# Performance work log

Measured on AMD Instinct MI355X. Metric: run time of the kernel, lower is better.

## Reference

```python
import jax, jax.numpy as jnp
import numpy as np

B, N_SNPS, N_GENES = 16, 500000, 20000
N_NODES, N_EDGES = 600000, 320000
NF, L = 8, 2
BN_EPS = 1e-5

def bn(x, g, b):
    # eval-mode BatchNorm1d with freshly-initialized running stats (mean=0, var=1)
    return x * jax.lax.rsqrt(jnp.float32(1.0) + BN_EPS) * g + b

def gelu(x):
    return jax.nn.gelu(x, approximate=False)  # torch F.gelu default (erf)

def setup_inputs():
    key = jax.random.key(0)
    ks = iter(jax.random.split(key, 40))
    nk = lambda: next(ks)
    lin = lambda kk, i, o: jax.random.normal(kk, (i, o), jnp.float32) * 0.02
    gam = lambda kk, n: 1.0 + 0.02 * jax.random.normal(kk, (n,), jnp.float32)
    inp = {}
    inp['snp'] = jax.random.uniform(nk(), (B, N_SNPS), jnp.float32)
    inp['snp_ids'] = jax.random.randint(nk(), (N_NODES,), 0, N_SNPS)
    inp['gene_of_node'] = jnp.sort(jax.random.randint(nk(), (N_NODES,), 0, N_GENES))
    inp['edge_src'] = jax.random.randint(nk(), (N_EDGES,), 0, N_GENES)
    inp['edge_dst'] = jax.random.randint(nk(), (N_EDGES,), 0, N_GENES)
    inp['filters'] = jax.random.normal(nk(), (NF, N_SNPS), jnp.float32) * 0.001
    inp['eps'] = jnp.zeros((L,), jnp.float32)  # GIN learn_eps, init 0
    inp['W1'] = jnp.stack([lin(nk(), NF, 2 * NF) for _ in range(L)])
    inp['b1'] = jnp.zeros((L, 2 * NF), jnp.float32)
    inp['g1'] = jnp.stack([gam(nk(), 2 * NF) for _ in range(L)])
    inp['bt1'] = jnp.zeros((L, 2 * NF), jnp.float32)
    inp['W2'] = jnp.stack([lin(nk(), 2 * NF, NF) for _ in range(L)])
    inp['b2'] = jnp.zeros((L, NF), jnp.float32)
    inp['g2'] = jnp.stack([gam(nk(), NF) for _ in range(L)])
    inp['bt2'] = jnp.zeros((L, NF), jnp.float32)
    inp['Wk'] = lin(nk(), NF, NF); inp['bk'] = jnp.zeros((NF,), jnp.float32)
    inp['Wq'] = lin(nk(), NF, 1)
    inp['Wv'] = lin(nk(), NF, NF); inp['bv'] = jnp.zeros((NF,), jnp.float32)
    inp['Wp1'] = lin(nk(), NF, 64); inp['bp1'] = jnp.zeros((64,), jnp.float32)
    inp['gp1'] = gam(nk(), 64); inp['btp1'] = jnp.zeros((64,), jnp.float32)
    inp['Wp2'] = lin(nk(), 64, 16); inp['bp2'] = jnp.zeros((16,), jnp.float32)
    inp['gp2'] = gam(nk(), 16); inp['btp2'] = jnp.zeros((16,), jnp.float32)
    inp['Wp3'] = lin(nk(), 16, 1); inp['bp3'] = jnp.zeros((1,), jnp.float32)
    return inp

def reference(snp, snp_ids, gene_of_node, edge_src, edge_dst, filters, eps,
              W1, b1, g1, bt1, W2, b2, g2, bt2,
              Wk, bk, Wq, Wv, bv,
              Wp1, bp1, gp1, btp1, Wp2, bp2, gp2, btp2, Wp3, bp3):
    # snp_h[b,n,f] = snp[b,n] * filters[f,n]  (concat of per-filter einsum 'bnd,n->bnd' with d=1)
    snp_h = snp[:, :, None] * filters.T[None]                      # [B, N_SNPS, NF]
    node_h = jnp.take(snp_h, snp_ids, axis=1)                      # [B, N_NODES, NF] gather per sample
    seg_gene = lambda x: jax.ops.segment_sum(x, gene_of_node, num_segments=N_GENES)
    h = jax.vmap(seg_gene)(node_h)                                 # [B, N_GENES, NF] SNP->gene readout
    seg_edge = lambda x: jax.ops.segment_sum(jnp.take(x, edge_src, axis=0), edge_dst, num_segments=N_GENES)
    for l in range(L):
        agg = jax.vmap(seg_edge)(h)                                # GIN sum aggregation on gene graph
        z = (1.0 + eps[l]) * h + agg
        z = gelu(bn(z @ W1[l] + b1[l], g1[l], bt1[l]))
        z = z @ W2[l] + b2[l]
        h = gelu(bn(z, g2[l], bt2[l]))
    # attentive readout: w = sigmoid(Wq(key(h))); graph feature = sum_nodes(value(h) * w)
    keys = h @ Wk + bk
    w = jax.nn.sigmoid(keys @ Wq)                                  # [B, N_GENES, 1]
    v = h @ Wv + bv
    g_h = jnp.sum(v * w, axis=1)                                   # [B, NF]
    z = gelu(bn(g_h @ Wp1 + bp1, gp1, btp1))
    z = gelu(bn(z @ Wp2 + bp2, gp2, btp2))
    preds = z @ Wp3 + bp3                                          # [B, 1]
    return preds, filters, w
```

## Files before the change

### kernel.cpp

```cpp
#include <hip/hip_runtime.h>
#include <math.h>

#define NSNPS  500000
#define NGENES 20000
#define NNODES 600000
#define NEDGES 320000
#define BB     16
#define NFILT  8
#define NBLK2  5000
#define MAXDEG 64

#define BN_SCALE 0.99999500003749968f

typedef unsigned short u16;

__device__ __forceinline__ float gelu_erf(float x) {
    return 0.5f * x * (1.0f + erff(x * 0.70710678118654752f));
}
__device__ __forceinline__ float sigmoidf_(float x) {
    return 1.0f / (1.0f + expf(-x));
}
__device__ __forceinline__ u16 f2bf(float x) {
    unsigned u = __float_as_uint(x);
    u += 0x7fffu + ((u >> 16) & 1u);
    return (u16)(u >> 16);
}
__device__ __forceinline__ float bf1(u16 v)      { return __uint_as_float(((unsigned)v) << 16); }
__device__ __forceinline__ float bflo(unsigned v){ return __uint_as_float(v << 16); }
__device__ __forceinline__ float bfhi(unsigned v){ return __uint_as_float(v & 0xffff0000u); }
__device__ __forceinline__ unsigned pack2(float a, float b) {
    return (unsigned)f2bf(a) | ((unsigned)f2bf(b) << 16);
}

#define KA_NA 1954
#define KA_NB 79
__global__ __launch_bounds__(256) void kA_prep(const float* __restrict__ snp,
                                               const float* __restrict__ filters,
                                               const int* __restrict__ gene_of_node,
                                               u16* __restrict__ nodeRow,
                                               float* __restrict__ out_filt,
                                               int* __restrict__ node_off,
                                               int* __restrict__ cursor,
                                               float* __restrict__ g_h8) {
    int bid = blockIdx.x;
    int t = threadIdx.x;

    if (bid < KA_NA) {
        int n = bid * 256 + t;
        if (n < NSNPS) {
            float f0 = filters[0 * NSNPS + n], f1 = filters[1 * NSNPS + n];
            float f2 = filters[2 * NSNPS + n], f3 = filters[3 * NSNPS + n];
            float f4 = filters[4 * NSNPS + n], f5 = filters[5 * NSNPS + n];
            float f6 = filters[6 * NSNPS + n], f7 = filters[7 * NSNPS + n];
            out_filt[0 * NSNPS + n] = f0; out_filt[1 * NSNPS + n] = f1;
            out_filt[2 * NSNPS + n] = f2; out_filt[3 * NSNPS + n] = f3;
            out_filt[4 * NSNPS + n] = f4; out_filt[5 * NSNPS + n] = f5;
            out_filt[6 * NSNPS + n] = f6; out_filt[7 * NSNPS + n] = f7;
            uint4 r0, r1, r2;
            r0.x = pack2(snp[0 * (size_t)NSNPS + n],  snp[1 * (size_t)NSNPS + n]);
            r0.y = pack2(snp[2 * (size_t)NSNPS + n],  snp[3 * (size_t)NSNPS + n]);
            r0.z = pack2(snp[4 * (size_t)NSNPS + n],  snp[5 * (size_t)NSNPS + n]);
            r0.w = pack2(snp[6 * (size_t)NSNPS + n],  snp[7 * (size_t)NSNPS + n]);
            r1.x = pack2(snp[8 * (size_t)NSNPS + n],  snp[9 * (size_t)NSNPS + n]);
            r1.y = pack2(snp[10 * (size_t)NSNPS + n], snp[11 * (size_t)NSNPS + n]);
            r1.z = pack2(snp[12 * (size_t)NSNPS + n], snp[13 * (size_t)NSNPS + n]);
            r1.w = pack2(snp[14 * (size_t)NSNPS + n], snp[15 * (size_t)NSNPS + n]);
            r2.x = pack2(f0, f1); r2.y = pack2(f2, f3);
            r2.z = pack2(f4, f5); r2.w = pack2(f6, f7);
            uint4* dst = (uint4*)(nodeRow + (size_t)n * 32);
            dst[0] = r0; dst[1] = r1; dst[2] = r2;
        }
        return;
    }
    int g = (bid - KA_NA) * 256 + t;
    if (g <= NGENES) {
        int lo = 0, hi = NNODES;
        while (lo < hi) {
            int mid = (lo + hi) >> 1;
            if (gene_of_node[mid] < g) lo = mid + 1; else hi = mid;
        }
        node_off[g] = lo;
    }
    if (g < NGENES) cursor[g] = g * MAXDEG;
    if (g < 1024)   g_h8[g] = 0.0f;
}

#define KB_SCAT 1250
#define KB_GATH 5000
__global__ __launch_bounds__(256) void kB_gather(const u16* __restrict__ nodeRow,
                                                 const int* __restrict__ snp_ids,
                                                 const int* __restrict__ node_off,
                                                 const int* __restrict__ edge_src,
                                                 const int* __restrict__ edge_dst,
                                                 int* __restrict__ cursor,
                                                 int* __restrict__ csr_src,
                                                 u16* __restrict__ h_bf) {
    int bid = blockIdx.x;
    int t = threadIdx.x;
    if (bid < KB_SCAT) {
        int e = bid * 256 + t;
        if (e < NEDGES) {
            int dst = edge_dst[e];
            int p = atomicAdd(&cursor[dst], 1);
            if (p < dst * MAXDEG + MAXDEG)
                csr_src[p] = edge_src[e];
        }
        return;
    }
    int wave = t >> 6, lane = t & 63;
    int g = (bid - KB_SCAT) * 4 + wave;
    int slot = lane >> 4;
    int b = lane & 15;
    int s = node_off[g], e = node_off[g + 1];

    float acc[8];
    #pragma unroll
    for (int f = 0; f < 8; f++) acc[f] = 0.0f;

    int i = s + slot;
    for (; i + 12 < e; i += 16) {
        int id0 = snp_ids[i];
        int id1 = snp_ids[i + 4];
        int id2 = snp_ids[i + 8];
        int id3 = snp_ids[i + 12];
        const u16* r0 = nodeRow + (size_t)id0 * 32;
        const u16* r1 = nodeRow + (size_t)id1 * 32;
        const u16* r2 = nodeRow + (size_t)id2 * 32;
        const u16* r3 = nodeRow + (size_t)id3 * 32;
        float v0 = bf1(r0[b]);
        float v1 = bf1(r1[b]);
        float v2 = bf1(r2[b]);
        float v3 = bf1(r3[b]);
        uint4 F0 = *(const uint4*)(r0 + 16);
        uint4 F1 = *(const uint4*)(r1 + 16);
        uint4 F2 = *(const uint4*)(r2 + 16);
        uint4 F3 = *(const uint4*)(r3 + 16);
        acc[0] += (v0 * bflo(F0.x) + v1 * bflo(F1.x)) + (v2 * bflo(F2.x) + v3 * bflo(F3.x));
        acc[1] += (v0 * bfhi(F0.x) + v1 * bfhi(F1.x)) + (v2 * bfhi(F2.x) + v3 * bfhi(F3.x));
        acc[2] += (v0 * bflo(F0.y) + v1 * bflo(F1.y)) + (v2 * bflo(F2.y) + v3 * bflo(F3.y));
        acc[3] += (v0 * bfhi(F0.y) + v1 * bfhi(F1.y)) + (v2 * bfhi(F2.y) + v3 * bfhi(F3.y));
        acc[4] += (v0 * bflo(F0.z) + v1 * bflo(F1.z)) + (v2 * bflo(F2.z) + v3 * bflo(F3.z));
        acc[5] += (v0 * bfhi(F0.z) + v1 * bfhi(F1.z)) + (v2 * bfhi(F2.z) + v3 * bfhi(F3.z));
        acc[6] += (v0 * bflo(F0.w) + v1 * bflo(F1.w)) + (v2 * bflo(F2.w) + v3 * bflo(F3.w));
        acc[7] += (v0 * bfhi(F0.w) + v1 * bfhi(F1.w)) + (v2 * bfhi(F2.w) + v3 * bfhi(F3.w));
    }
    for (; i + 4 < e; i += 8) {
        int id0 = snp_ids[i];
        int id1 = snp_ids[i + 4];
        const u16* r0 = nodeRow + (size_t)id0 * 32;
        const u16* r1 = nodeRow + (size_t)id1 * 32;
        float v0 = bf1(r0[b]);
        float v1 = bf1(r1[b]);
        uint4 F0 = *(const uint4*)(r0 + 16);
        uint4 F1 = *(const uint4*)(r1 + 16);
        acc[0] += v0 * bflo(F0.x) + v1 * bflo(F1.x);
        acc[1] += v0 * bfhi(F0.x) + v1 * bfhi(F1.x);
        acc[2] += v0 * bflo(F0.y) + v1 * bflo(F1.y);
        acc[3] += v0 * bfhi(F0.y) + v1 * bfhi(F1.y);
        acc[4] += v0 * bflo(F0.z) + v1 * bflo(F1.z);
        acc[5] += v0 * bfhi(F0.z) + v1 * bfhi(F1.z);
        acc[6] += v0 * bflo(F0.w) + v1 * bflo(F1.w);
        acc[7] += v0 * bfhi(F0.w) + v1 * bfhi(F1.w);
    }
    if (i < e) {
        int id0 = snp_ids[i];
        const u16* r0 = nodeRow + (size_t)id0 * 32;
        float v0 = bf1(r0[b]);
        uint4 F0 = *(const uint4*)(r0 + 16);
        acc[0] += v0 * bflo(F0.x); acc[1] += v0 * bfhi(F0.x);
        acc[2] += v0 * bflo(F0.y); acc[3] += v0 * bfhi(F0.y);
        acc[4] += v0 * bflo(F0.z); acc[5] += v0 * bfhi(F0.z);
        acc[6] += v0 * bflo(F0.w); acc[7] += v0 * bfhi(F0.w);
    }
    #pragma unroll
    for (int f = 0; f < 8; f++) {
        acc[f] += __shfl_xor(acc[f], 16, 64);
        acc[f] += __shfl_xor(acc[f], 32, 64);
    }
    if (lane < 16) {
        uint4 o;
        o.x = pack2(acc[0], acc[1]); o.y = pack2(acc[2], acc[3]);
        o.z = pack2(acc[4], acc[5]); o.w = pack2(acc[6], acc[7]);
        *(uint4*)(h_bf + (size_t)g * 128 + lane * 8) = o;
    }
}

__global__ __launch_bounds__(256) void kC_gin1(const u16* __restrict__ hin,
                                               u16* __restrict__ hout,
                                               const int* __restrict__ cursor,
                                               const int* __restrict__ csr_src,
                                               const float* __restrict__ eps_l,
                                               const float* __restrict__ W1,
                                               const float* __restrict__ b1,
                                               const float* __restrict__ g1,
                                               const float* __restrict__ bt1,
                                               const float* __restrict__ W2,
                                               const float* __restrict__ b2,
                                               const float* __restrict__ g2,
                                               const float* __restrict__ bt2) {
    __shared__ float sW1[128], sb1[16], sg1[16], sbt1[16];
    __shared__ float sW2[128], sb2[8], sg2[8], sbt2[8];
    int t = threadIdx.x;
    if (t < 128) { sW1[t] = W1[t]; sW2[t] = W2[t]; }
    if (t < 16)  { sb1[t] = b1[t]; sg1[t] = g1[t]; sbt1[t] = bt1[t]; }
    if (t < 8)   { sb2[t] = b2[t]; sg2[t] = g2[t]; sbt2[t] = bt2[t]; }

    int chunk = blockIdx.x & 3;
    int g = (blockIdx.x >> 2) * 16 + (t >> 4);
    int u = t & 15;
    int half = u >> 3;
    int colpos = u & 7;
    int fh = colpos & 1;
    int jgroup = half * 2 + fh;
    int col = chunk * 32 + colpos * 4;
    const u16* __restrict__ hc = hin + col;
    float epsv = 1.0f + eps_l[0];

    float a0, a1, a2, a3;
    if (half == 0) {
        uint2 su = *(const uint2*)(hc + (size_t)g * 128);
        a0 = bflo(su.x) * epsv; a1 = bfhi(su.x) * epsv;
        a2 = bflo(su.y) * epsv; a3 = bfhi(su.y) * epsv;
    } else {
        a0 = a1 = a2 = a3 = 0.0f;
    }

    int s = g * MAXDEG;
    int e = cursor[g];
    e = (e < s + MAXDEG) ? e : (s + MAXDEG);
    int k = s + half;
    for (; k + 14 < e; k += 16) {
        int i0 = csr_src[k],      i1 = csr_src[k + 2];
        int i2 = csr_src[k + 4],  i3 = csr_src[k + 6];
        int i4 = csr_src[k + 8],  i5 = csr_src[k + 10];
        int i6 = csr_src[k + 12], i7 = csr_src[k + 14];
        uint2 v0 = *(const uint2*)(hc + (size_t)i0 * 128);
        uint2 v1 = *(const uint2*)(hc + (size_t)i1 * 128);
        uint2 v2 = *(const uint2*)(hc + (size_t)i2 * 128);
        uint2 v3 = *(const uint2*)(hc + (size_t)i3 * 128);
        uint2 v4 = *(const uint2*)(hc + (size_t)i4 * 128);
        uint2 v5 = *(const uint2*)(hc + (size_t)i5 * 128);
        uint2 v6 = *(const uint2*)(hc + (size_t)i6 * 128);
        uint2 v7 = *(const uint2*)(hc + (size_t)i7 * 128);
        a0 += ((bflo(v0.x) + bflo(v1.x)) + (bflo(v2.x) + bflo(v3.x)))
            + ((bflo(v4.x) + bflo(v5.x)) + (bflo(v6.x) + bflo(v7.x)));
        a1 += ((bfhi(v0.x) + bfhi(v1.x)) + (bfhi(v2.x) + bfhi(v3.x)))
            + ((bfhi(v4.x) + bfhi(v5.x)) + (bfhi(v6.x) + bfhi(v7.x)));
        a2 += ((bflo(v0.y) + bflo(v1.y)) + (bflo(v2.y) + bflo(v3.y)))
            + ((bflo(v4.y) + bflo(v5.y)) + (bflo(v6.y) + bflo(v7.y)));
        a3 += ((bfhi(v0.y) + bfhi(v1.y)) + (bfhi(v2.y) + bfhi(v3.y)))
            + ((bfhi(v4.y) + bfhi(v5.y)) + (bfhi(v6.y) + bfhi(v7.y)));
    }
    for (; k < e; k += 2) {
        int i0 = csr_src[k];
        uint2 v0 = *(const uint2*)(hc + (size_t)i0 * 128);
        a0 += bflo(v0.x); a1 += bfhi(v0.x);
        a2 += bflo(v0.y); a3 += bfhi(v0.y);
    }
    __syncthreads();

    a0 += __shfl_xor(a0, 8, 64);
    a1 += __shfl_xor(a1, 8, 64);
    a2 += __shfl_xor(a2, 8, 64);
    a3 += __shfl_xor(a3, 8, 64);
    float p0 = __shfl_xor(a0, 1, 64);
    float p1 = __shfl_xor(a1, 1, 64);
    float p2 = __shfl_xor(a2, 1, 64);
    float p3 = __shfl_xor(a3, 1, 64);
    float z[8];
    z[fh * 4 + 0] = a0; z[fh * 4 + 1] = a1; z[fh * 4 + 2] = a2; z[fh * 4 + 3] = a3;
    z[(1 - fh) * 4 + 0] = p0; z[(1 - fh) * 4 + 1] = p1;
    z[(1 - fh) * 4 + 2] = p2; z[(1 - fh) * 4 + 3] = p3;

    float op[8];
    #pragma unroll
    for (int f = 0; f < 8; f++) op[f] = (jgroup == 0) ? sb2[f] : 0.0f;
    #pragma unroll
    for (int jj = 0; jj < 4; jj++) {
        int j = jgroup * 4 + jj;
        float s1 = sb1[j];
        #pragma unroll
        for (int i2 = 0; i2 < 8; i2++) s1 += z[i2] * sW1[i2 * 16 + j];
        s1 = s1 * BN_SCALE * sg1[j] + sbt1[j];
        s1 = gelu_erf(s1);
        #pragma unroll
        for (int f = 0; f < 8; f++) op[f] += s1 * sW2[j * 8 + f];
    }
    float r[4];
    #pragma unroll
    for (int fi = 0; fi < 4; fi++) {
        int f = fh * 4 + fi;
        float x = op[f] + __shfl_xor(op[f], 1, 64);
        x += __shfl_xor(x, 8, 64);
        r[fi] = gelu_erf(x * BN_SCALE * sg2[f] + sbt2[f]);
    }
    if (half == 0) {
        uint2 ou;
        ou.x = pack2(r[0], r[1]); ou.y = pack2(r[2], r[3]);
        *(uint2*)(hout + (size_t)g * 128 + col) = ou;
    }
}

__global__ __launch_bounds__(256) void kD_gin2(const u16* __restrict__ hin,
                                               const int* __restrict__ cursor,
                                               const int* __restrict__ csr_src,
                                               const float* __restrict__ eps_l,
                                               const float* __restrict__ W1,
                                               const float* __restrict__ b1,
                                               const float* __restrict__ g1,
                                               const float* __restrict__ bt1,
                                               const float* __restrict__ W2,
                                               const float* __restrict__ b2,
                                               const float* __restrict__ g2,
                                               const float* __restrict__ bt2,
                                               const float* __restrict__ Wk,
                                               const float* __restrict__ bk,
                                               const float* __restrict__ Wq,
                                               const float* __restrict__ Wv,
                                               const float* __restrict__ bv,
                                               float* __restrict__ w_out,
                                               float* __restrict__ g_h8) {
    __shared__ float sW1[128], sb1[16], sg1[16], sbt1[16];
    __shared__ float sW2[128], sb2[8], sg2[8], sbt2[8];
    __shared__ float sWk[64], sWv[64], sbk[8], sbv[8], sWq[8];
    __shared__ float sRed[4][4][8];
    int t = threadIdx.x;
    if (t < 128) { sW1[t] = W1[t]; sW2[t] = W2[t]; }
    if (t < 64)  { sWk[t] = Wk[t]; sWv[t] = Wv[t]; }
    if (t < 16)  { sb1[t] = b1[t]; sg1[t] = g1[t]; sbt1[t] = bt1[t]; }
    if (t < 8)   { sb2[t] = b2[t]; sg2[t] = g2[t]; sbt2[t] = bt2[t];
                   sbk[t] = bk[t]; sbv[t] = bv[t]; sWq[t] = Wq[t]; }

    int chunk = blockIdx.x & 3;
    int g = (blockIdx.x >> 2) * 16 + (t >> 4);
    int u = t & 15;
    int half = u >> 3;
    int colpos = u & 7;
    int fh = colpos & 1;
    int jgroup = half * 2 + fh;
    int b = chunk * 4 + (colpos >> 1);
    int col = chunk * 32 + colpos * 4;
    const u16* __restrict__ hc = hin + col;
    float epsv = 1.0f + eps_l[0];

    float a0, a1, a2, a3;
    if (half == 0) {
        uint2 su = *(const uint2*)(hc + (size_t)g * 128);
        a0 = bflo(su.x) * epsv; a1 = bfhi(su.x) * epsv;
        a2 = bflo(su.y) * epsv; a3 = bfhi(su.y) * epsv;
    } else {
        a0 = a1 = a2 = a3 = 0.0f;
    }

    int s = g * MAXDEG;
    int e = cursor[g];
    e = (e < s + MAXDEG) ? e : (s + MAXDEG);
    int k = s + half;
    for (; k + 14 < e; k += 16) {
        int i0 = csr_src[k],      i1 = csr_src[k + 2];
        int i2 = csr_src[k + 4],  i3 = csr_src[k + 6];
        int i4 = csr_src[k + 8],  i5 = csr_src[k + 10];
        int i6 = csr_src[k + 12], i7 = csr_src[k + 14];
        uint2 v0 = *(const uint2*)(hc + (size_t)i0 * 128);
        uint2 v1 = *(const uint2*)(hc + (size_t)i1 * 128);
        uint2 v2 = *(const uint2*)(hc + (size_t)i2 * 128);
        uint2 v3 = *(const uint2*)(hc + (size_t)i3 * 128);
        uint2 v4 = *(const uint2*)(hc + (size_t)i4 * 128);
        uint2 v5 = *(const uint2*)(hc + (size_t)i5 * 128);
        uint2 v6 = *(const uint2*)(hc + (size_t)i6 * 128);
        uint2 v7 = *(const uint2*)(hc + (size_t)i7 * 128);
        a0 += ((bflo(v0.x) + bflo(v1.x)) + (bflo(v2.x) + bflo(v3.x)))
            + ((bflo(v4.x) + bflo(v5.x)) + (bflo(v6.x) + bflo(v7.x)));
        a1 += ((bfhi(v0.x) + bfhi(v1.x)) + (bfhi(v2.x) + bfhi(v3.x)))
            + ((bfhi(v4.x) + bfhi(v5.x)) + (bfhi(v6.x) + bfhi(v7.x)));
        a2 += ((bflo(v0.y) + bflo(v1.y)) + (bflo(v2.y) + bflo(v3.y)))
            + ((bflo(v4.y) + bflo(v5.y)) + (bflo(v6.y) + bflo(v7.y)));
        a3 += ((bfhi(v0.y) + bfhi(v1.y)) + (bfhi(v2.y) + bfhi(v3.y)))
            + ((bfhi(v4.y) + bfhi(v5.y)) + (bfhi(v6.y) + bfhi(v7.y)));
    }
    for (; k < e; k += 2) {
        int i0 = csr_src[k];
        uint2 v0 = *(const uint2*)(hc + (size_t)i0 * 128);
        a0 += bflo(v0.x); a1 += bfhi(v0.x);
        a2 += bflo(v0.y); a3 += bfhi(v0.y);
    }
    __syncthreads();

    a0 += __shfl_xor(a0, 8, 64);
    a1 += __shfl_xor(a1, 8, 64);
    a2 += __shfl_xor(a2, 8, 64);
    a3 += __shfl_xor(a3, 8, 64);
    float p0 = __shfl_xor(a0, 1, 64);
    float p1 = __shfl_xor(a1, 1, 64);
    float p2 = __shfl_xor(a2, 1, 64);
    float p3 = __shfl_xor(a3, 1, 64);
    float z[8];
    z[fh * 4 + 0] = a0; z[fh * 4 + 1] = a1; z[fh * 4 + 2] = a2; z[fh * 4 + 3] = a3;
    z[(1 - fh) * 4 + 0] = p0; z[(1 - fh) * 4 + 1] = p1;
    z[(1 - fh) * 4 + 2] = p2; z[(1 - fh) * 4 + 3] = p3;

    float op[8];
    #pragma unroll
    for (int f = 0; f < 8; f++) op[f] = (jgroup == 0) ? sb2[f] : 0.0f;
    #pragma unroll
    for (int jj = 0; jj < 4; jj++) {
        int j = jgroup * 4 + jj;
        float s1 = sb1[j];
        #pragma unroll
        for (int i2 = 0; i2 < 8; i2++) s1 += z[i2] * sW1[i2 * 16 + j];
        s1 = s1 * BN_SCALE * sg1[j] + sbt1[j];
        s1 = gelu_erf(s1);
        #pragma unroll
        for (int f = 0; f < 8; f++) op[f] += s1 * sW2[j * 8 + f];
    }
    float hvh[4];
    #pragma unroll
    for (int fi = 0; fi < 4; fi++) {
        int f = fh * 4 + fi;
        float x = op[f] + __shfl_xor(op[f], 1, 64);
        x += __shfl_xor(x, 8, 64);
        hvh[fi] = gelu_erf(x * BN_SCALE * sg2[f] + sbt2[f]);
    }
    float hv[8];
    #pragma unroll
    for (int fi = 0; fi < 4; fi++) {
        hv[fh * 4 + fi] = hvh[fi];
        hv[(1 - fh) * 4 + fi] = __shfl_xor(hvh[fi], 1, 64);
    }

    float qp = 0.0f;
    #pragma unroll
    for (int jj = 0; jj < 2; jj++) {
        int j = jgroup * 2 + jj;
        float key = sbk[j];
        #pragma unroll
        for (int i2 = 0; i2 < 8; i2++) key += hv[i2] * sWk[i2 * 8 + j];
        qp += key * sWq[j];
    }
    float q = qp + __shfl_xor(qp, 1, 64);
    q += __shfl_xor(q, 8, 64);
    float w = sigmoidf_(q);
    if (fh == 0 && half == 0) w_out[(size_t)b * NGENES + g] = w;

    float contrib[4];
    #pragma unroll
    for (int fi = 0; fi < 4; fi++) {
        int f = fh * 4 + fi;
        float v = sbv[f];
        #pragma unroll
        for (int i2 = 0; i2 < 8; i2++) v += hv[i2] * sWv[i2 * 8 + f];
        contrib[fi] = (half == 0) ? v * w : 0.0f;
    }
    #pragma unroll
    for (int fi = 0; fi < 4; fi++) {
        contrib[fi] += __shfl_xor(contrib[fi], 8, 64);
        contrib[fi] += __shfl_xor(contrib[fi], 16, 64);
        contrib[fi] += __shfl_xor(contrib[fi], 32, 64);
    }
    int wave = t >> 6, lane = t & 63;
    if (lane < 8) {
        #pragma unroll
        for (int fi = 0; fi < 4; fi++)
            sRed[wave][lane >> 1][(lane & 1) * 4 + fi] = contrib[fi];
    }
    __syncthreads();
    if (t < 32) {
        int bl = t >> 3, f = t & 7;
        float sm = sRed[0][bl][f] + sRed[1][bl][f] + sRed[2][bl][f] + sRed[3][bl][f];
        int shard = (blockIdx.x >> 2) & 7;
        atomicAdd(&g_h8[shard * 128 + (chunk * 4 + bl) * 8 + f], sm);
    }
}

__global__ __launch_bounds__(1024) void kE_head(const float* __restrict__ g_h8,
                                                const float* __restrict__ Wp1, const float* __restrict__ bp1,
                                                const float* __restrict__ gp1, const float* __restrict__ btp1,
                                                const float* __restrict__ Wp2, const float* __restrict__ bp2,
                                                const float* __restrict__ gp2, const float* __restrict__ btp2,
                                                const float* __restrict__ Wp3, const float* __restrict__ bp3,
                                                float* __restrict__ preds) {
    __shared__ float sgh[128];
    __shared__ float z1[16 * 64];
    __shared__ float z2[16 * 16];
    int t = threadIdx.x;
    if (t < 128) {
        float s01 = g_h8[t]           + g_h8[128 + t];
        float s23 = g_h8[256 + t]     + g_h8[384 + t];
        float s45 = g_h8[512 + t]     + g_h8[640 + t];
        float s67 = g_h8[768 + t]     + g_h8[896 + t];
        sgh[t] = (s01 + s23) + (s45 + s67);
    }
    __syncthreads();
    {
        int b = t >> 6, j = t & 63;
        float s = bp1[j];
        #pragma unroll
        for (int k = 0; k < 8; k++) s += sgh[b * 8 + k] * Wp1[k * 64 + j];
        s = s * BN_SCALE * gp1[j] + btp1[j];
        z1[b * 64 + j] = gelu_erf(s);
    }
    __syncthreads();
    if (t < 256) {
        int b = t >> 4, j = t & 15;
        float s = bp2[j];
        for (int k = 0; k < 64; k++) s += z1[b * 64 + k] * Wp2[k * 16 + j];
        s = s * BN_SCALE * gp2[j] + btp2[j];
        z2[b * 16 + j] = gelu_erf(s);
    }
    __syncthreads();
    if (t < 16) {
        float s = bp3[0];
        #pragma unroll
        for (int k = 0; k < 16; k++) s += z2[t * 16 + k] * Wp3[k];
        preds[t] = s;
    }
}

extern "C" void kernel_launch(void* const* d_in, const int* in_sizes, int n_in,
                              void* d_out, int out_size, void* d_ws, size_t ws_size,
                              hipStream_t stream) {
    const float* snp          = (const float*)d_in[0];
    const int*   snp_ids      = (const int*)  d_in[1];
    const int*   gene_of_node = (const int*)  d_in[2];
    const int*   edge_src     = (const int*)  d_in[3];
    const int*   edge_dst     = (const int*)  d_in[4];
    const float* filters      = (const float*)d_in[5];
    const float* eps          = (const float*)d_in[6];
    const float* W1  = (const float*)d_in[7];
    const float* b1  = (const float*)d_in[8];
    const float* g1  = (const float*)d_in[9];
    const float* bt1 = (const float*)d_in[10];
    const float* W2  = (const float*)d_in[11];
    const float* b2  = (const float*)d_in[12];
    const float* g2  = (const float*)d_in[13];
    const float* bt2 = (const float*)d_in[14];
    const float* Wk  = (const float*)d_in[15];
    const float* bk  = (const float*)d_in[16];
    const float* Wq  = (const float*)d_in[17];
    const float* Wv  = (const float*)d_in[18];
    const float* bv  = (const float*)d_in[19];
    const float* Wp1 = (const float*)d_in[20];
    const float* bp1 = (const float*)d_in[21];
    const float* gp1 = (const float*)d_in[22];
    const float* btp1= (const float*)d_in[23];
    const float* Wp2 = (const float*)d_in[24];
    const float* bp2 = (const float*)d_in[25];
    const float* gp2 = (const float*)d_in[26];
    const float* btp2= (const float*)d_in[27];
    const float* Wp3 = (const float*)d_in[28];
    const float* bp3 = (const float*)d_in[29];

    float* out        = (float*)d_out;
    float* out_preds  = out;
    float* out_filt   = out + 16;
    float* out_w      = out + 16 + NFILT * NSNPS;

    char* ws = (char*)d_ws;
    size_t off = 0;
    u16* nodeRow = (u16*)(ws + off); off += (size_t)NSNPS * 64;
    u16* h0   = (u16*)(ws + off); off += (size_t)NGENES * 128 * 2;
    u16* h1   = (u16*)(ws + off); off += (size_t)NGENES * 128 * 2;
    int* node_off = (int*)(ws + off); off += ((NGENES + 1) * 4 + 255) / 256 * 256;
    int* cursor   = (int*)(ws + off); off += (NGENES * 4 + 255) / 256 * 256;
    int* csr_src  = (int*)(ws + off); off += (size_t)NGENES * MAXDEG * 4;
    float* g_h8   = (float*)(ws + off); off += 8 * 128 * 4;

    kA_prep<<<KA_NA + KA_NB, 256, 0, stream>>>(
        snp, filters, gene_of_node, nodeRow, out_filt, node_off, cursor, g_h8);
    kB_gather<<<KB_SCAT + KB_GATH, 256, 0, stream>>>(
        nodeRow, snp_ids, node_off, edge_src, edge_dst, cursor, csr_src, h0);
    kC_gin1<<<NBLK2, 256, 0, stream>>>(h0, h1, cursor, csr_src, eps + 0,
                                       W1 + 0 * 128, b1 + 0 * 16, g1 + 0 * 16, bt1 + 0 * 16,
                                       W2 + 0 * 128, b2 + 0 * 8, g2 + 0 * 8, bt2 + 0 * 8);
    kD_gin2<<<NBLK2, 256, 0, stream>>>(h1, cursor, csr_src, eps + 1,
                                       W1 + 1 * 128, b1 + 1 * 16, g1 + 1 * 16, bt1 + 1 * 16,
                                       W2 + 1 * 128, b2 + 1 * 8, g2 + 1 * 8, bt2 + 1 * 8,
                                       Wk, bk, Wq, Wv, bv, out_w, g_h8);
    kE_head<<<1, 1024, 0, stream>>>(g_h8, Wp1, bp1, gp1, btp1,
                                    Wp2, bp2, gp2, btp2, Wp3, bp3, out_preds);
}
```

Baseline: 261.4 us.

## Fuse head into last GIN kernel via last-block atomic, move filter copy

Removes the separate single-block head kernel: each GIN-2 block bumps an atomic counter, and the last block to finish reads the reduced graph features and runs the prediction MLP. The filters passthrough copy moves from the prep kernel into extra blocks of the GIN-2 launch, so it can overlap with the gather-heavy work. The GELU epilogue is also changed so each lane evaluates only two erf-GELUs and exchanges results by shuffle, instead of four redundant ones. The cost is an added atomic and vmcnt wait per block, a serial tail in the last block, and more shared memory per block in GIN-2, which may reduce occupancy.

Measured after the change: 304.9 us. +16.6%, slower.

```diff
diff --git a/kernel.cpp b/kernel.cpp
--- a/kernel.cpp
+++ b/kernel.cpp
@@ -38,10 +38,10 @@
                                                const float* __restrict__ filters,
                                                const int* __restrict__ gene_of_node,
                                                u16* __restrict__ nodeRow,
-                                               float* __restrict__ out_filt,
                                                int* __restrict__ node_off,
                                                int* __restrict__ cursor,
-                                               float* __restrict__ g_h8) {
+                                               float* __restrict__ g_h8,
+                                               unsigned* __restrict__ done) {
     int bid = blockIdx.x;
     int t = threadIdx.x;
 
@@ -52,10 +52,6 @@
             float f2 = filters[2 * NSNPS + n], f3 = filters[3 * NSNPS + n];
             float f4 = filters[4 * NSNPS + n], f5 = filters[5 * NSNPS + n];
             float f6 = filters[6 * NSNPS + n], f7 = filters[7 * NSNPS + n];
-            out_filt[0 * NSNPS + n] = f0; out_filt[1 * NSNPS + n] = f1;
-            out_filt[2 * NSNPS + n] = f2; out_filt[3 * NSNPS + n] = f3;
-            out_filt[4 * NSNPS + n] = f4; out_filt[5 * NSNPS + n] = f5;
-            out_filt[6 * NSNPS + n] = f6; out_filt[7 * NSNPS + n] = f7;
             uint4 r0, r1, r2;
             r0.x = pack2(snp[0 * (size_t)NSNPS + n],  snp[1 * (size_t)NSNPS + n]);
             r0.y = pack2(snp[2 * (size_t)NSNPS + n],  snp[3 * (size_t)NSNPS + n]);
@@ -83,6 +79,7 @@
     }
     if (g < NGENES) cursor[g] = g * MAXDEG;
     if (g < 1024)   g_h8[g] = 0.0f;
+    if (g == 0)     *done = 0u;
 }
 
 #define KB_SCAT 1250
@@ -286,17 +283,23 @@
         #pragma unroll
         for (int f = 0; f < 8; f++) op[f] += s1 * sW2[j * 8 + f];
     }
-    float r[4];
-    #pragma unroll
-    for (int fi = 0; fi < 4; fi++) {
-        int f = fh * 4 + fi;
-        float x = op[f] + __shfl_xor(op[f], 1, 64);
-        x += __shfl_xor(x, 8, 64);
-        r[fi] = gelu_erf(x * BN_SCALE * sg2[f] + sbt2[f]);
-    }
+    int f0 = fh * 4;
+    float x, xs0, xs1, xs2, xs3;
+    x = op[f0 + 0] + __shfl_xor(op[f0 + 0], 1, 64); x += __shfl_xor(x, 8, 64);
+    xs0 = x * BN_SCALE * sg2[f0 + 0] + sbt2[f0 + 0];
+    x = op[f0 + 1] + __shfl_xor(op[f0 + 1], 1, 64); x += __shfl_xor(x, 8, 64);
+    xs1 = x * BN_SCALE * sg2[f0 + 1] + sbt2[f0 + 1];
+    x = op[f0 + 2] + __shfl_xor(op[f0 + 2], 1, 64); x += __shfl_xor(x, 8, 64);
+    xs2 = x * BN_SCALE * sg2[f0 + 2] + sbt2[f0 + 2];
+    x = op[f0 + 3] + __shfl_xor(op[f0 + 3], 1, 64); x += __shfl_xor(x, 8, 64);
+    xs3 = x * BN_SCALE * sg2[f0 + 3] + sbt2[f0 + 3];
+    float ga = gelu_erf(half ? xs2 : xs0);
+    float gb = gelu_erf(half ? xs3 : xs1);
+    float oa = __shfl_xor(ga, 8, 64);
+    float ob = __shfl_xor(gb, 8, 64);
     if (half == 0) {
         uint2 ou;
-        ou.x = pack2(r[0], r[1]); ou.y = pack2(r[2], r[3]);
+        ou.x = pack2(ga, gb); ou.y = pack2(oa, ob);
         *(uint2*)(hout + (size_t)g * 128 + col) = ou;
     }
 }
@@ -319,20 +322,50 @@
                                                const float* __restrict__ Wv,
                                                const float* __restrict__ bv,
                                                float* __restrict__ w_out,
-                                               float* __restrict__ g_h8) {
+                                               float* __restrict__ g_h8,
+                                               const float* __restrict__ filters,
+                                               float* __restrict__ out_filt,
+                                               const float* __restrict__ Wp1, const float* __restrict__ bp1,
+                                               const float* __restrict__ gp1, const float* __restrict__ btp1,
+                                               const float* __restrict__ Wp2, const float* __restrict__ bp2,
+                                               const float* __restrict__ gp2, const float* __restrict__ btp2,
+                                               const float* __restrict__ Wp3, const float* __restrict__ bp3,
+                                               float* __restrict__ preds,
+                                               unsigned* __restrict__ done) {
     __shared__ float sW1[128], sb1[16], sg1[16], sbt1[16];
     __shared__ float sW2[128], sb2[8], sg2[8], sbt2[8];
     __shared__ float sWk[64], sWv[64], sbk[8], sbv[8], sWq[8];
     __shared__ float sRed[4][4][8];
+    __shared__ float sgh[128];
+    __shared__ float z1[1024];
+    __shared__ float z2[256];
+    __shared__ unsigned sLast;
+    int bid = blockIdx.x;
     int t = threadIdx.x;
+
+    if (bid >= NBLK2) {
+        int n = (bid - NBLK2) * 256 + t;
+        if (n < NSNPS) {
+            out_filt[0 * NSNPS + n] = filters[0 * NSNPS + n];
+            out_filt[1 * NSNPS + n] = filters[1 * NSNPS + n];
+            out_filt[2 * NSNPS + n] = filters[2 * NSNPS + n];
+            out_filt[3 * NSNPS + n] = filters[3 * NSNPS + n];
+            out_filt[4 * NSNPS + n] = filters[4 * NSNPS + n];
+            out_filt[5 * NSNPS + n] = filters[5 * NSNPS + n];
+            out_filt[6 * NSNPS + n] = filters[6 * NSNPS + n];
+            out_filt[7 * NSNPS + n] = filters[7 * NSNPS + n];
+        }
+        return;
+    }
+
     if (t < 128) { sW1[t] = W1[t]; sW2[t] = W2[t]; }
     if (t < 64)  { sWk[t] = Wk[t]; sWv[t] = Wv[t]; }
     if (t < 16)  { sb1[t] = b1[t]; sg1[t] = g1[t]; sbt1[t] = bt1[t]; }
     if (t < 8)   { sb2[t] = b2[t]; sg2[t] = g2[t]; sbt2[t] = bt2[t];
                    sbk[t] = bk[t]; sbv[t] = bv[t]; sWq[t] = Wq[t]; }
 
-    int chunk = blockIdx.x & 3;
-    int g = (blockIdx.x >> 2) * 16 + (t >> 4);
+    int chunk = bid & 3;
+    int g = (bid >> 2) * 16 + (t >> 4);
     int u = t & 15;
     int half = u >> 3;
     int colpos = u & 7;
@@ -413,14 +446,25 @@
         #pragma unroll
         for (int f = 0; f < 8; f++) op[f] += s1 * sW2[j * 8 + f];
     }
+    int f0 = fh * 4;
+    float x, xs0, xs1, xs2, xs3;
+    x = op[f0 + 0] + __shfl_xor(op[f0 + 0], 1, 64); x += __shfl_xor(x, 8, 64);
+    xs0 = x * BN_SCALE * sg2[f0 + 0] + sbt2[f0 + 0];
+    x = op[f0 + 1] + __shfl_xor(op[f0 + 1], 1, 64); x += __shfl_xor(x, 8, 64);
+    xs1 = x * BN_SCALE * sg2[f0 + 1] + sbt2[f0 + 1];
+    x = op[f0 + 2] + __shfl_xor(op[f0 + 2], 1, 64); x += __shfl_xor(x, 8, 64);
+    xs2 = x * BN_SCALE * sg2[f0 + 2] + sbt2[f0 + 2];
+    x = op[f0 + 3] + __shfl_xor(op[f0 + 3], 1, 64); x += __shfl_xor(x, 8, 64);
+    xs3 = x * BN_SCALE * sg2[f0 + 3] + sbt2[f0 + 3];
+    float ga = gelu_erf(half ? xs2 : xs0);
+    float gb = gelu_erf(half ? xs3 : xs1);
+    float oa = __shfl_xor(ga, 8, 64);
+    float ob = __shfl_xor(gb, 8, 64);
     float hvh[4];
-    #pragma unroll
-    for (int fi = 0; fi < 4; fi++) {
-        int f = fh * 4 + fi;
-        float x = op[f] + __shfl_xor(op[f], 1, 64);
-        x += __shfl_xor(x, 8, 64);
-        hvh[fi] = gelu_erf(x * BN_SCALE * sg2[f] + sbt2[f]);
-    }
+    hvh[0] = half ? oa : ga;
+    hvh[1] = half ? ob : gb;
+    hvh[2] = half ? ga : oa;
+    hvh[3] = half ? gb : ob;
     float hv[8];
     #pragma unroll
     for (int fi = 0; fi < 4; fi++) {
@@ -467,52 +511,55 @@
     if (t < 32) {
         int bl = t >> 3, f = t & 7;
         float sm = sRed[0][bl][f] + sRed[1][bl][f] + sRed[2][bl][f] + sRed[3][bl][f];
-        int shard = (blockIdx.x >> 2) & 7;
+        int shard = (bid >> 2) & 7;
         atomicAdd(&g_h8[shard * 128 + (chunk * 4 + bl) * 8 + f], sm);
     }
-}
-
-__global__ __launch_bounds__(1024) void kE_head(const float* __restrict__ g_h8,
-                                                const float* __restrict__ Wp1, const float* __restrict__ bp1,
-                                                const float* __restrict__ gp1, const float* __restrict__ btp1,
-                                                const float* __restrict__ Wp2, const float* __restrict__ bp2,
-                                                const float* __restrict__ gp2, const float* __restrict__ btp2,
-                                                const float* __restrict__ Wp3, const float* __restrict__ bp3,
-                                                float* __restrict__ preds) {
-    __shared__ float sgh[128];
-    __shared__ float z1[16 * 64];
-    __shared__ float z2[16 * 16];
-    int t = threadIdx.x;
+
+    asm volatile("s_waitcnt vmcnt(0)" ::: "memory");
+    __syncthreads();
+    if (t == 0) {
+        unsigned old = __hip_atomic_fetch_add(done, 1u, __ATOMIC_RELAXED, __HIP_MEMORY_SCOPE_AGENT);
+        sLast = ((old % (unsigned)NBLK2) == (unsigned)(NBLK2 - 1)) ? 1u : 0u;
+    }
+    __syncthreads();
+    if (!sLast) return;
+
     if (t < 128) {
-        float s01 = g_h8[t]           + g_h8[128 + t];
-        float s23 = g_h8[256 + t]     + g_h8[384 + t];
-        float s45 = g_h8[512 + t]     + g_h8[640 + t];
-        float s67 = g_h8[768 + t]     + g_h8[896 + t];
+        float s01 = __hip_atomic_load(&g_h8[t],       __ATOMIC_RELAXED, __HIP_MEMORY_SCOPE_AGENT)
+                  + __hip_atomic_load(&g_h8[128 + t], __ATOMIC_RELAXED, __HIP_MEMORY_SCOPE_AGENT);
+        float s23 = __hip_atomic_load(&g_h8[256 + t], __ATOMIC_RELAXED, __HIP_MEMORY_SCOPE_AGENT)
+                  + __hip_atomic_load(&g_h8[384 + t], __ATOMIC_RELAXED, __HIP_MEMORY_SCOPE_AGENT);
+        float s45 = __hip_atomic_load(&g_h8[512 + t], __ATOMIC_RELAXED, __HIP_MEMORY_SCOPE_AGENT)
+                  + __hip_atomic_load(&g_h8[640 + t], __ATOMIC_RELAXED, __HIP_MEMORY_SCOPE_AGENT);
+        float s67 = __hip_atomic_load(&g_h8[768 + t], __ATOMIC_RELAXED, __HIP_MEMORY_SCOPE_AGENT)
+                  + __hip_atomic_load(&g_h8[896 + t], __ATOMIC_RELAXED, __HIP_MEMORY_SCOPE_AGENT);
         sgh[t] = (s01 + s23) + (s45 + s67);
     }
     __syncthreads();
+    #pragma unroll
+    for (int r = 0; r < 4; r++) {
+        int idx = r * 256 + t;
+        int bb = idx >> 6, j = idx & 63;
+        float s2 = bp1[j];
+        #pragma unroll
+        for (int kk = 0; kk < 8; kk++) s2 += sgh[bb * 8 + kk] * Wp1[kk * 64 + j];
+        s2 = s2 * BN_SCALE * gp1[j] + btp1[j];
+        z1[idx] = gelu_erf(s2);
+    }
+    __syncthreads();
     {
-        int b = t >> 6, j = t & 63;
-        float s = bp1[j];
-        #pragma unroll
-        for (int k = 0; k < 8; k++) s += sgh[b * 8 + k] * Wp1[k * 64 + j];
-        s = s * BN_SCALE * gp1[j] + btp1[j];
-        z1[b * 64 + j] = gelu_erf(s);
-    }
-    __syncthreads();
-    if (t < 256) {
-        int b = t >> 4, j = t & 15;
-        float s = bp2[j];
-        for (int k = 0; k < 64; k++) s += z1[b * 64 + k] * Wp2[k * 16 + j];
-        s = s * BN_SCALE * gp2[j] + btp2[j];
-        z2[b * 16 + j] = gelu_erf(s);
+        int bb = t >> 4, j = t & 15;
+        float s2 = bp2[j];
+        for (int kk = 0; kk < 64; kk++) s2 += z1[bb * 64 + kk] * Wp2[kk * 16 + j];
+        s2 = s2 * BN_SCALE * gp2[j] + btp2[j];
+        z2[t] = gelu_erf(s2);
     }
     __syncthreads();
     if (t < 16) {
-        float s = bp3[0];
-        #pragma unroll
-        for (int k = 0; k < 16; k++) s += z2[t * 16 + k] * Wp3[k];
-        preds[t] = s;
+        float s2 = bp3[0];
+        #pragma unroll
+        for (int kk = 0; kk < 16; kk++) s2 += z2[t * 16 + kk] * Wp3[kk];
+        preds[t] = s2;
     }
 }
 
@@ -564,18 +611,21 @@
     int* cursor   = (int*)(ws + off); off += (NGENES * 4 + 255) / 256 * 256;
     int* csr_src  = (int*)(ws + off); off += (size_t)NGENES * MAXDEG * 4;
     float* g_h8   = (float*)(ws + off); off += 8 * 128 * 4;
+    unsigned* done= (unsigned*)(ws + off); off += 256;
 
     kA_prep<<<KA_NA + KA_NB, 256, 0, stream>>>(
-        snp, filters, gene_of_node, nodeRow, out_filt, node_off, cursor, g_h8);
+        snp, filters, gene_of_node, nodeRow, node_off, cursor, g_h8, done);
     kB_gather<<<KB_SCAT + KB_GATH, 256, 0, stream>>>(
         nodeRow, snp_ids, node_off, edge_src, edge_dst, cursor, csr_src, h0);
     kC_gin1<<<NBLK2, 256, 0, stream>>>(h0, h1, cursor, csr_src, eps + 0,
                                        W1 + 0 * 128, b1 + 0 * 16, g1 + 0 * 16, bt1 + 0 * 16,
                                        W2 + 0 * 128, b2 + 0 * 8, g2 + 0 * 8, bt2 + 0 * 8);
-    kD_gin2<<<NBLK2, 256, 0, stream>>>(h1, cursor, csr_src, eps + 1,
-                                       W1 + 1 * 128, b1 + 1 * 16, g1 + 1 * 16, bt1 + 1 * 16,
-                                       W2 + 1 * 128, b2 + 1 * 8, g2 + 1 * 8, bt2 + 1 * 8,
-                                       Wk, bk, Wq, Wv, bv, out_w, g_h8);
-    kE_head<<<1, 1024, 0, stream>>>(g_h8, Wp1, bp1, gp1, btp1,
-                                    Wp2, bp2, gp2, btp2, Wp3, bp3, out_preds);
-}
+    kD_gin2<<<NBLK2 + KA_NA, 256, 0, stream>>>(
+        h1, cursor, csr_src, eps + 1,
+        W1 + 1 * 128, b1 + 1 * 16, g1 + 1 * 16, bt1 + 1 * 16,
+        W2 + 1 * 128, b2 + 1 * 8, g2 + 1 * 8, bt2 + 1 * 8,
+        Wk, bk, Wq, Wv, bv, out_w, g_h8,
+        filters, out_filt,
+        Wp1, bp1, gp1, btp1, Wp2, bp2, gp2, btp2, Wp3, bp3,
+        out_preds, done);
+}
```
